# Performance work log

Measured on AMD Instinct MI355X. Metric: run time of the kernel, lower is better.

## Reference

```python
import jax, jax.numpy as jnp
import numpy as np

N_NODES = 10000
N_EDGES = 160000
IN_C, HID_C, OUT_C = 256, 512, 256
DROP_P = 0.5


def setup_inputs() -> dict:
    key = jax.random.key(0)
    ks = jax.random.split(key, 6)
    tensor = jax.random.normal(ks[0], (N_NODES, IN_C), dtype=jnp.float32)
    edge_index = jax.random.randint(ks[1], (2, N_EDGES), 0, N_NODES, dtype=jnp.int64)
    # Glorot-ish init for GCNConv linear weights, zero bias (PyG default bias init is zeros)
    W1 = jax.random.normal(ks[2], (IN_C, HID_C), dtype=jnp.float32) * (1.0 / np.sqrt(IN_C))
    b1 = jnp.zeros((HID_C,), dtype=jnp.float32)
    W2 = jax.random.normal(ks[3], (HID_C, OUT_C), dtype=jnp.float32) * (1.0 / np.sqrt(HID_C))
    b2 = jnp.zeros((OUT_C,), dtype=jnp.float32)
    return {"tensor": tensor, "edge_index": edge_index, "W1": W1, "b1": b1, "W2": W2, "b2": b2}


def _gcn_layer(x, W, b, src, dst, n_nodes):
    # x' = D^{-1/2} (A + I) D^{-1/2} X W + b  (PyG GCNConv, add_self_loops=True)
    xw = x @ W                                             # [N, C_out]
    deg = jax.ops.segment_sum(jnp.ones(src.shape[0], xw.dtype), dst,
                              num_segments=n_nodes)        # includes self-loops -> deg >= 1
    dinv = jax.lax.rsqrt(deg)
    norm = dinv[src] * dinv[dst]                           # [E+N]
    msg = xw[src] * norm[:, None]                          # gather + normalize
    out = jax.ops.segment_sum(msg, dst, num_segments=n_nodes)  # scatter-add
    return out + b


def _dropout(x, key, p):
    keep = jax.random.bernoulli(key, 1.0 - p, x.shape)
    return jnp.where(keep, x / (1.0 - p), jnp.zeros((), x.dtype))


def reference(tensor, edge_index, W1, b1, W2, b2):
    n = tensor.shape[0]
    src, dst = edge_index[0], edge_index[1]
    loops = jnp.arange(n, dtype=src.dtype)
    src_f = jnp.concatenate([src, loops])
    dst_f = jnp.concatenate([dst, loops])

    dk1, dk2 = jax.random.split(jax.random.key(42))
    h = _gcn_layer(tensor, W1, b1, src_f, dst_f, n)
    h = jax.nn.relu(h)
    h = _dropout(h, dk1, DROP_P)
    h = _gcn_layer(h, W2, b2, src_f, dst_f, n)
    h = jax.nn.relu(h)
    h = _dropout(h, dk2, DROP_P)
    return h
```

## Files before the change

kernel.cpp:

```cpp
#include <hip/hip_runtime.h>
#include <stdint.h>


#define C_IN 256
#define C_HID 512
#define C_OUT 256

typedef unsigned short ushort_t;
typedef __bf16 bf16x8 __attribute__((ext_vector_type(8)));
typedef float floatx4 __attribute__((ext_vector_type(4)));

__host__ __device__ __forceinline__ void tf_rounds(unsigned& x0, unsigned& x1,
                                                   unsigned k0, unsigned k1) {
  unsigned k2 = k0 ^ k1 ^ 0x1BD11BDAu;
#define ROT(r) { x0 += x1; x1 = (x1 << r) | (x1 >> (32 - r)); x1 ^= x0; }
  x0 += k0; x1 += k1;
  ROT(13) ROT(15) ROT(26) ROT(6)
  x0 += k1; x1 += k2 + 1u;
  ROT(17) ROT(29) ROT(16) ROT(24)
  x0 += k2; x1 += k0 + 2u;
  ROT(13) ROT(15) ROT(26) ROT(6)
  x0 += k0; x1 += k1 + 3u;
  ROT(17) ROT(29) ROT(16) ROT(24)
  x0 += k1; x1 += k2 + 4u;
  ROT(13) ROT(15) ROT(26) ROT(6)
  x0 += k2; x1 += k0 + 5u;
#undef ROT
}

__device__ __forceinline__ float drop_scale(unsigned j, unsigned k0, unsigned k1) {
  unsigned x0 = 0u, x1 = j;
  tf_rounds(x0, x1, k0, k1);
  unsigned bits = x0 ^ x1;
  float u = __uint_as_float((bits >> 9) | 0x3f800000u) - 1.0f;
  return (u < 0.5f) ? 2.0f : 0.0f;
}

__device__ __forceinline__ ushort_t f2bf(float f) {
  unsigned u = __float_as_uint(f);
  unsigned r = (u + 0x7fffu + ((u >> 16) & 1u)) >> 16;
  return (ushort_t)r;
}
__device__ __forceinline__ float bf2f(ushort_t h) {
  return __uint_as_float(((unsigned)h) << 16);
}

__global__ __launch_bounds__(256) void k_detect(const unsigned* __restrict__ raw,
                                                unsigned* flag, int nwords) {
  __shared__ unsigned sh[256];
  unsigned acc = 0;
  for (int i = 1 + 2 * (int)threadIdx.x; i < nwords; i += 512) acc |= raw[i];
  sh[threadIdx.x] = acc;
  __syncthreads();
  for (int s = 128; s > 0; s >>= 1) {
    if ((int)threadIdx.x < s) sh[threadIdx.x] |= sh[threadIdx.x + s];
    __syncthreads();
  }
  if (threadIdx.x == 0) *flag = (sh[0] == 0u) ? 1u : 0u;
}

__global__ __launch_bounds__(256) void k_zero(int* p, int n) {
  int i = blockIdx.x * 256 + threadIdx.x;
  if (i < n) p[i] = 0;
}

__global__ __launch_bounds__(256) void k_convert(const void* __restrict__ raw,
                                                 const unsigned* __restrict__ flag,
                                                 int* __restrict__ eic,
                                                 int* __restrict__ cnt,
                                                 int E) {
  int i = blockIdx.x * 256 + threadIdx.x;
  if (i >= 2 * E) return;
  int v;
  if (*flag) v = (int)((const long long*)raw)[i];
  else       v = ((const int*)raw)[i];
  eic[i] = v;
  if (i >= E) atomicAdd(&cnt[v], 1);
}

__global__ __launch_bounds__(256) void k_scan_a(const int* __restrict__ cnt,
                                                int* __restrict__ bsum, int n) {
  __shared__ int sh[256];
  int i = blockIdx.x * 256 + threadIdx.x;
  sh[threadIdx.x] = (i < n) ? cnt[i] : 0;
  __syncthreads();
  for (int s = 128; s > 0; s >>= 1) {
    if ((int)threadIdx.x < s) sh[threadIdx.x] += sh[threadIdx.x + s];
    __syncthreads();
  }
  if (threadIdx.x == 0) bsum[blockIdx.x] = sh[0];
}
__global__ __launch_bounds__(64) void k_scan_b(const int* __restrict__ bsum,
                                               int* __restrict__ boff,
                                               int* __restrict__ roff_last,
                                               int nb) {
  if (threadIdx.x == 0) {
    int run = 0;
    for (int b = 0; b < nb; ++b) { boff[b] = run; run += bsum[b]; }
    *roff_last = run;
  }
}
__global__ __launch_bounds__(256) void k_scan_c(const int* __restrict__ cnt,
                                                const int* __restrict__ boff,
                                                int* __restrict__ roff,
                                                int* __restrict__ cursor,
                                                float* __restrict__ dinv, int n) {
  __shared__ int sh[256];
  int i = blockIdx.x * 256 + threadIdx.x;
  int v = (i < n) ? cnt[i] : 0;
  sh[threadIdx.x] = v;
  __syncthreads();
  for (int s = 1; s < 256; s <<= 1) {
    int t = ((int)threadIdx.x >= s) ? sh[threadIdx.x - s] : 0;
    __syncthreads();
    sh[threadIdx.x] += t;
    __syncthreads();
  }
  if (i < n) {
    int excl = boff[blockIdx.x] + sh[threadIdx.x] - v;
    roff[i] = excl;
    cursor[i] = excl;
    dinv[i] = rsqrtf((float)(v + 1));
  }
}

__global__ __launch_bounds__(256) void k_scatter(const int* __restrict__ eic,
                                                 int* __restrict__ cursor,
                                                 int* __restrict__ csr, int E) {
  int e = blockIdx.x * 256 + threadIdx.x;
  if (e >= E) return;
  int s = eic[e], d = eic[E + e];
  int slot = atomicAdd(&cursor[d], 1);
  csr[slot] = s;
}

__global__ __launch_bounds__(256) void k_wconv2(const float* __restrict__ W1,
                                                const float* __restrict__ W2,
                                                ushort_t* __restrict__ h1,
                                                ushort_t* __restrict__ l1,
                                                ushort_t* __restrict__ h2,
                                                ushort_t* __restrict__ l2) {
  int idx = blockIdx.x * 256 + threadIdx.x;
  const int S1 = C_IN * C_HID;
  const float* W; ushort_t *hi, *lo; int K, Nn, li;
  if (idx < S1) { W = W1; hi = h1; lo = l1; K = C_IN; Nn = C_HID; li = idx; }
  else { W = W2; hi = h2; lo = l2; K = C_HID; Nn = C_OUT; li = idx - S1; }
  int k = li / Nn, n = li - k * Nn;
  float v = W[li];
  ushort_t h = f2bf(v);
  hi[(size_t)n * K + k] = h;
  lo[(size_t)n * K + k] = f2bf(v - bf2f(h));
}

template <int EPI>
__global__ __launch_bounds__(256) void k_gather4(const int* __restrict__ roff,
                                                 const int* __restrict__ csr,
                                                 const float* __restrict__ dinv,
                                                 const float* __restrict__ x,
                                                 const float* __restrict__ bias,
                                                 void* __restrict__ o1,
                                                 void* __restrict__ o2,
                                                 unsigned dk0, unsigned dk1) {
  int g = threadIdx.x >> 6;
  int tg = threadIdx.x & 63;
  int node = blockIdx.x * 4 + g;
  float dd = dinv[node];
  float4 v = ((const float4*)(x + (size_t)node * 256))[tg];
  float4 acc = make_float4(dd * v.x, dd * v.y, dd * v.z, dd * v.w);
  int p = roff[node], end = roff[node + 1];
  for (; p + 4 <= end; p += 4) {
    int s0 = csr[p], s1 = csr[p + 1], s2 = csr[p + 2], s3 = csr[p + 3];
    float w0 = dinv[s0], w1 = dinv[s1], w2 = dinv[s2], w3 = dinv[s3];
    float4 a = ((const float4*)(x + (size_t)s0 * 256))[tg];
    float4 b = ((const float4*)(x + (size_t)s1 * 256))[tg];
    float4 c = ((const float4*)(x + (size_t)s2 * 256))[tg];
    float4 d = ((const float4*)(x + (size_t)s3 * 256))[tg];
    acc.x += w0 * a.x + w1 * b.x + w2 * c.x + w3 * d.x;
    acc.y += w0 * a.y + w1 * b.y + w2 * c.y + w3 * d.y;
    acc.z += w0 * a.z + w1 * b.z + w2 * c.z + w3 * d.z;
    acc.w += w0 * a.w + w1 * b.w + w2 * c.w + w3 * d.w;
  }
  for (; p < end; ++p) {
    int s0 = csr[p];
    float w0 = dinv[s0];
    float4 a = ((const float4*)(x + (size_t)s0 * 256))[tg];
    acc.x += w0 * a.x; acc.y += w0 * a.y; acc.z += w0 * a.z; acc.w += w0 * a.w;
  }
  acc.x *= dd; acc.y *= dd; acc.z *= dd; acc.w *= dd;
  if (EPI) {
    float4 bb = ((const float4*)bias)[tg];
    acc.x = fmaxf(acc.x + bb.x, 0.0f);
    acc.y = fmaxf(acc.y + bb.y, 0.0f);
    acc.z = fmaxf(acc.z + bb.z, 0.0f);
    acc.w = fmaxf(acc.w + bb.w, 0.0f);
    unsigned jb = (unsigned)node * 256u + (unsigned)tg * 4u;
    acc.x *= drop_scale(jb + 0u, dk0, dk1);
    acc.y *= drop_scale(jb + 1u, dk0, dk1);
    acc.z *= drop_scale(jb + 2u, dk0, dk1);
    acc.w *= drop_scale(jb + 3u, dk0, dk1);
    ((float4*)o1)[(size_t)node * 64 + tg] = acc;
  } else {
    ushort_t h0 = f2bf(acc.x), h1 = f2bf(acc.y), h2 = f2bf(acc.z), h3 = f2bf(acc.w);
    ushort4 hv = make_ushort4(h0, h1, h2, h3);
    ushort4 lv = make_ushort4(f2bf(acc.x - bf2f(h0)), f2bf(acc.y - bf2f(h1)),
                              f2bf(acc.z - bf2f(h2)), f2bf(acc.w - bf2f(h3)));
    ((ushort4*)o1)[(size_t)node * 64 + tg] = hv;
    ((ushort4*)o2)[(size_t)node * 64 + tg] = lv;
  }
}

template <int EPI>
__global__ __launch_bounds__(256) void k_gemm3(
    const ushort_t* __restrict__ Ahi, const ushort_t* __restrict__ Alo,
    const ushort_t* __restrict__ Bhi, const ushort_t* __restrict__ Blo,
    const float* __restrict__ bias,
    ushort_t* __restrict__ Chi, ushort_t* __restrict__ Clo,
    float* __restrict__ Cf,
    int M, int N, int K, unsigned dk0, unsigned dk1) {
  __shared__ ushort_t sAh[128 * 32], sAl[128 * 32], sBh[128 * 32], sBl[128 * 32];
  const int t = threadIdx.x;
  const int lane = t & 63, wave = t >> 6;
  const int wm = wave & 1, wn = wave >> 1;
  const int quad = lane >> 4, l16 = lane & 15;
  const int row0 = blockIdx.y * 128, col0 = blockIdx.x * 128;
  const int srow = t >> 2;
  const int skc = (t & 3) * 8;

  floatx4 acc[4][4] = {};

  const int ra0 = min(row0 + srow, M - 1);
  const int ra1 = min(row0 + 64 + srow, M - 1);
  const int rb0 = col0 + srow;
  const int rb1 = col0 + 64 + srow;

  for (int kt = 0; kt < K; kt += 32) {
    const size_t ka = (size_t)kt + skc;
    uint4 vA0h = *(const uint4*)(Ahi + (size_t)ra0 * K + ka);
    uint4 vA1h = *(const uint4*)(Ahi + (size_t)ra1 * K + ka);
    uint4 vA0l = *(const uint4*)(Alo + (size_t)ra0 * K + ka);
    uint4 vA1l = *(const uint4*)(Alo + (size_t)ra1 * K + ka);
    uint4 vB0h = *(const uint4*)(Bhi + (size_t)rb0 * K + ka);
    uint4 vB1h = *(const uint4*)(Bhi + (size_t)rb1 * K + ka);
    uint4 vB0l = *(const uint4*)(Blo + (size_t)rb0 * K + ka);
    uint4 vB1l = *(const uint4*)(Blo + (size_t)rb1 * K + ka);
    __syncthreads();
    *(uint4*)&sAh[srow * 32 + skc] = vA0h;
    *(uint4*)&sAh[(64 + srow) * 32 + skc] = vA1h;
    *(uint4*)&sAl[srow * 32 + skc] = vA0l;
    *(uint4*)&sAl[(64 + srow) * 32 + skc] = vA1l;
    *(uint4*)&sBh[srow * 32 + skc] = vB0h;
    *(uint4*)&sBh[(64 + srow) * 32 + skc] = vB1h;
    *(uint4*)&sBl[srow * 32 + skc] = vB0l;
    *(uint4*)&sBl[(64 + srow) * 32 + skc] = vB1l;
    __syncthreads();

    bf16x8 ah[4], al[4], bh[4], bl[4];
#pragma unroll
    for (int i = 0; i < 4; ++i) {
      int off = (wm * 64 + i * 16 + l16) * 32 + quad * 8;
      ah[i] = *(const bf16x8*)&sAh[off];
      al[i] = *(const bf16x8*)&sAl[off];
    }
#pragma unroll
    for (int j = 0; j < 4; ++j) {
      int off = (wn * 64 + j * 16 + l16) * 32 + quad * 8;
      bh[j] = *(const bf16x8*)&sBh[off];
      bl[j] = *(const bf16x8*)&sBl[off];
    }
#pragma unroll
    for (int i = 0; i < 4; ++i)
#pragma unroll
      for (int j = 0; j < 4; ++j) {
        acc[i][j] = __builtin_amdgcn_mfma_f32_16x16x32_bf16(ah[i], bh[j], acc[i][j], 0, 0, 0);
        acc[i][j] = __builtin_amdgcn_mfma_f32_16x16x32_bf16(ah[i], bl[j], acc[i][j], 0, 0, 0);
        acc[i][j] = __builtin_amdgcn_mfma_f32_16x16x32_bf16(al[i], bh[j], acc[i][j], 0, 0, 0);
      }
  }

#pragma unroll
  for (int i = 0; i < 4; ++i) {
#pragma unroll
    for (int j = 0; j < 4; ++j) {
      int gc = col0 + wn * 64 + j * 16 + l16;
#pragma unroll
      for (int reg = 0; reg < 4; ++reg) {
        int gr = row0 + wm * 64 + i * 16 + quad * 4 + reg;
        if (gr >= M) continue;
        float v = acc[i][j][reg];
        size_t o = (size_t)gr * N + gc;
        if (EPI) {
          v += bias[gc];
          v = fmaxf(v, 0.0f);
          v *= drop_scale((unsigned)gr * (unsigned)N + (unsigned)gc, dk0, dk1);
          ushort_t h = f2bf(v);
          Chi[o] = h;
          Clo[o] = f2bf(v - bf2f(h));
        } else {
          Cf[o] = v;
        }
      }
    }
  }
}

extern "C" void kernel_launch(void* const* d_in, const int* in_sizes, int n_in,
                              void* d_out, int out_size, void* d_ws, size_t ws_size,
                              hipStream_t stream) {
  const float* x  = (const float*)d_in[0];
  const void*  ei = d_in[1];
  const float* W1 = (const float*)d_in[2];
  const float* b1 = (const float*)d_in[3];
  const float* W2 = (const float*)d_in[4];
  const float* b2 = (const float*)d_in[5];
  float* out = (float*)d_out;

  const int N = in_sizes[0] / C_IN;
  const int E = in_sizes[1] / 2;
  const int NB = (N + 255) / 256;

  unsigned a0 = 0u, a1 = 0u, b0 = 0u, b1k = 1u;
  tf_rounds(a0, a1, 0u, 42u);
  tf_rounds(b0, b1k, 0u, 42u);

  uintptr_t base = (uintptr_t)d_ws;
  unsigned*  flag   = (unsigned*)base;
  int*       bsum   = (int*)(base + 4096);
  int*       boff   = (int*)(base + 8192);
  int*       cnt    = (int*)(base + 16 * 1024);
  int*       roff   = (int*)(base + 64 * 1024);
  int*       cursor = (int*)(base + 128 * 1024);
  float*     dinv   = (float*)(base + 192 * 1024);
  int*       eic    = (int*)(base + 256 * 1024);
  int*       csr    = (int*)(base + 2u * 1024 * 1024);
  ushort_t*  Ahi    = (ushort_t*)(base + 4u  * 1024 * 1024);
  ushort_t*  Alo    = (ushort_t*)(base + 10u * 1024 * 1024);
  ushort_t*  H1hi   = (ushort_t*)(base + 16u * 1024 * 1024);
  ushort_t*  H1lo   = (ushort_t*)(base + 27u * 1024 * 1024);
  float*     hw2    = (float*)(base + 38u * 1024 * 1024);
  ushort_t*  W1thi  = (ushort_t*)(base + 49u * 1024 * 1024);
  ushort_t*  W1tlo  = (ushort_t*)(base + 49u * 1024 * 1024 + 512 * 1024);
  ushort_t*  W2thi  = (ushort_t*)(base + 50u * 1024 * 1024);
  ushort_t*  W2tlo  = (ushort_t*)(base + 50u * 1024 * 1024 + 512 * 1024);

  dim3 b256(256);
  k_detect<<<dim3(1), b256, 0, stream>>>((const unsigned*)ei, flag, 8192);
  k_zero<<<dim3(NB), b256, 0, stream>>>(cnt, N);
  k_convert<<<dim3((2 * E + 255) / 256), b256, 0, stream>>>(ei, flag, eic, cnt, E);
  k_scan_a<<<dim3(NB), b256, 0, stream>>>(cnt, bsum, N);
  k_scan_b<<<dim3(1), dim3(64), 0, stream>>>(bsum, boff, roff + N, NB);
  k_scan_c<<<dim3(NB), b256, 0, stream>>>(cnt, boff, roff, cursor, dinv, N);
  k_scatter<<<dim3((E + 255) / 256), b256, 0, stream>>>(eic, cursor, csr, E);
  k_wconv2<<<dim3((C_IN * C_HID + C_HID * C_OUT + 255) / 256), b256, 0, stream>>>(
      W1, W2, W1thi, W1tlo, W2thi, W2tlo);
  k_gather4<0><<<dim3(N / 4), b256, 0, stream>>>(roff, csr, dinv, x, nullptr,
                                                 Ahi, Alo, 0u, 0u);
  k_gemm3<1><<<dim3(C_HID / 128, (N + 127) / 128), b256, 0, stream>>>(
      Ahi, Alo, W1thi, W1tlo, b1, H1hi, H1lo, nullptr, N, C_HID, C_IN, a0, a1);
  k_gemm3<0><<<dim3(C_OUT / 128, (N + 127) / 128), b256, 0, stream>>>(
      H1hi, H1lo, W2thi, W2tlo, nullptr, nullptr, nullptr, hw2, N, C_OUT, C_HID, 0u, 0u);
  k_gather4<1><<<dim3(N / 4), b256, 0, stream>>>(roff, csr, dinv, hw2, b2,
                                                 out, nullptr, b0, b1k);
}
```

Before: 215.8 us.

## Merge setup kernels, single-block scan, and wave-shuffled CSR index loads in gather

Folds the zeroing into the detect kernel and the weight conversion into the CSR scatter kernel, and replaces the three-kernel scan with a single 1024-thread block scan, cutting the launch count from eight preprocessing kernels to four. The gather kernels now load up to 64 neighbor indices and weights cooperatively, one per lane, and broadcast them with shuffles instead of every lane reading them redundantly. The single-block scan only covers up to 16384 nodes, and the CSR scatter and weight conversion blocks now share one grid.

```diff
diff --git a/kernel.cpp b/kernel.cpp
--- a/kernel.cpp
+++ b/kernel.cpp
@@ -45,8 +45,15 @@
   return __uint_as_float(((unsigned)h) << 16);
 }
 
-__global__ __launch_bounds__(256) void k_detect(const unsigned* __restrict__ raw,
-                                                unsigned* flag, int nwords) {
+__global__ __launch_bounds__(256) void k_setup(const unsigned* __restrict__ raw,
+                                               unsigned* flag, int nwords,
+                                               int* __restrict__ cnt, int n,
+                                               int nb) {
+  if ((int)blockIdx.x < nb) {
+    int i = blockIdx.x * 256 + threadIdx.x;
+    if (i < n) cnt[i] = 0;
+    return;
+  }
   __shared__ unsigned sh[256];
   unsigned acc = 0;
   for (int i = 1 + 2 * (int)threadIdx.x; i < nwords; i += 512) acc |= raw[i];
@@ -57,11 +64,6 @@
     __syncthreads();
   }
   if (threadIdx.x == 0) *flag = (sh[0] == 0u) ? 1u : 0u;
-}
-
-__global__ __launch_bounds__(256) void k_zero(int* p, int n) {
-  int i = blockIdx.x * 256 + threadIdx.x;
-  if (i < n) p[i] = 0;
 }
 
 __global__ __launch_bounds__(256) void k_convert(const void* __restrict__ raw,
@@ -78,70 +80,65 @@
   if (i >= E) atomicAdd(&cnt[v], 1);
 }
 
-__global__ __launch_bounds__(256) void k_scan_a(const int* __restrict__ cnt,
-                                                int* __restrict__ bsum, int n) {
-  __shared__ int sh[256];
-  int i = blockIdx.x * 256 + threadIdx.x;
-  sh[threadIdx.x] = (i < n) ? cnt[i] : 0;
-  __syncthreads();
-  for (int s = 128; s > 0; s >>= 1) {
-    if ((int)threadIdx.x < s) sh[threadIdx.x] += sh[threadIdx.x + s];
-    __syncthreads();
-  }
-  if (threadIdx.x == 0) bsum[blockIdx.x] = sh[0];
-}
-__global__ __launch_bounds__(64) void k_scan_b(const int* __restrict__ bsum,
-                                               int* __restrict__ boff,
-                                               int* __restrict__ roff_last,
-                                               int nb) {
-  if (threadIdx.x == 0) {
-    int run = 0;
-    for (int b = 0; b < nb; ++b) { boff[b] = run; run += bsum[b]; }
-    *roff_last = run;
-  }
-}
-__global__ __launch_bounds__(256) void k_scan_c(const int* __restrict__ cnt,
-                                                const int* __restrict__ boff,
+#define SCAN_CH 16
+__global__ __launch_bounds__(1024) void k_scan1(const int* __restrict__ cnt,
                                                 int* __restrict__ roff,
                                                 int* __restrict__ cursor,
                                                 float* __restrict__ dinv, int n) {
-  __shared__ int sh[256];
-  int i = blockIdx.x * 256 + threadIdx.x;
-  int v = (i < n) ? cnt[i] : 0;
-  sh[threadIdx.x] = v;
+  __shared__ int sh[1024];
+  const int t = threadIdx.x;
+  const int base = t * SCAN_CH;
+  int vv[SCAN_CH], loc[SCAN_CH];
+  int sum = 0;
+#pragma unroll
+  for (int i = 0; i < SCAN_CH; ++i) {
+    int idx = base + i;
+    int v = (idx < n) ? cnt[idx] : 0;
+    vv[i] = v;
+    loc[i] = sum;
+    sum += v;
+  }
+  sh[t] = sum;
   __syncthreads();
-  for (int s = 1; s < 256; s <<= 1) {
-    int t = ((int)threadIdx.x >= s) ? sh[threadIdx.x - s] : 0;
-    __syncthreads();
-    sh[threadIdx.x] += t;
-    __syncthreads();
-  }
-  if (i < n) {
-    int excl = boff[blockIdx.x] + sh[threadIdx.x] - v;
-    roff[i] = excl;
-    cursor[i] = excl;
-    dinv[i] = rsqrtf((float)(v + 1));
-  }
-}
-
-__global__ __launch_bounds__(256) void k_scatter(const int* __restrict__ eic,
-                                                 int* __restrict__ cursor,
-                                                 int* __restrict__ csr, int E) {
-  int e = blockIdx.x * 256 + threadIdx.x;
-  if (e >= E) return;
-  int s = eic[e], d = eic[E + e];
-  int slot = atomicAdd(&cursor[d], 1);
-  csr[slot] = s;
-}
-
-__global__ __launch_bounds__(256) void k_wconv2(const float* __restrict__ W1,
-                                                const float* __restrict__ W2,
-                                                ushort_t* __restrict__ h1,
-                                                ushort_t* __restrict__ l1,
-                                                ushort_t* __restrict__ h2,
-                                                ushort_t* __restrict__ l2) {
-  int idx = blockIdx.x * 256 + threadIdx.x;
+  for (int s = 1; s < 1024; s <<= 1) {
+    int v = (t >= s) ? sh[t - s] : 0;
+    __syncthreads();
+    sh[t] += v;
+    __syncthreads();
+  }
+  int tex = sh[t] - sum;
+#pragma unroll
+  for (int i = 0; i < SCAN_CH; ++i) {
+    int idx = base + i;
+    if (idx < n) {
+      int excl = tex + loc[i];
+      roff[idx] = excl;
+      cursor[idx] = excl;
+      dinv[idx] = rsqrtf((float)(vv[i] + 1));
+    }
+  }
+  if (t == 1023) roff[n] = sh[1023];
+}
+
+__global__ __launch_bounds__(256) void k_scat_wconv(
+    const int* __restrict__ eic, int* __restrict__ cursor,
+    int* __restrict__ csr, int E, int SB,
+    const float* __restrict__ W1, const float* __restrict__ W2,
+    ushort_t* __restrict__ h1, ushort_t* __restrict__ l1,
+    ushort_t* __restrict__ h2, ushort_t* __restrict__ l2) {
+  int b = blockIdx.x;
+  if (b < SB) {
+    int e = b * 256 + threadIdx.x;
+    if (e >= E) return;
+    int s = eic[e], d = eic[E + e];
+    int slot = atomicAdd(&cursor[d], 1);
+    csr[slot] = s;
+    return;
+  }
+  int idx = (b - SB) * 256 + threadIdx.x;
   const int S1 = C_IN * C_HID;
+  const int S2 = C_HID * C_OUT;
+  if (idx >= S1 + S2) return;
   const float* W; ushort_t *hi, *lo; int K, Nn, li;
   if (idx < S1) { W = W1; hi = h1; lo = l1; K = C_IN; Nn = C_HID; li = idx; }
   else { W = W2; hi = h2; lo = l2; K = C_HID; Nn = C_OUT; li = idx - S1; }
@@ -161,51 +158,61 @@
                                                  void* __restrict__ o1,
                                                  void* __restrict__ o2,
                                                  unsigned dk0, unsigned dk1) {
-  int g = threadIdx.x >> 6;
-  int tg = threadIdx.x & 63;
-  int node = blockIdx.x * 4 + g;
+  const int g = threadIdx.x >> 6;
+  const int lane = threadIdx.x & 63;
+  const int node = blockIdx.x * 4 + g;
   float dd = dinv[node];
-  float4 v = ((const float4*)(x + (size_t)node * 256))[tg];
+  float4 v = ((const float4*)(x + (size_t)node * 256))[lane];
   float4 acc = make_float4(dd * v.x, dd * v.y, dd * v.z, dd * v.w);
   int p = roff[node], end = roff[node + 1];
-  for (; p + 4 <= end; p += 4) {
-    int s0 = csr[p], s1 = csr[p + 1], s2 = csr[p + 2], s3 = csr[p + 3];
-    float w0 = dinv[s0], w1 = dinv[s1], w2 = dinv[s2], w3 = dinv[s3];
-    float4 a = ((const float4*)(x + (size_t)s0 * 256))[tg];
-    float4 b = ((const float4*)(x + (size_t)s1 * 256))[tg];
-    float4 c = ((const float4*)(x + (size_t)s2 * 256))[tg];
-    float4 d = ((const float4*)(x + (size_t)s3 * 256))[tg];
-    acc.x += w0 * a.x + w1 * b.x + w2 * c.x + w3 * d.x;
-    acc.y += w0 * a.y + w1 * b.y + w2 * c.y + w3 * d.y;
-    acc.z += w0 * a.z + w1 * b.z + w2 * c.z + w3 * d.z;
-    acc.w += w0 * a.w + w1 * b.w + w2 * c.w + w3 * d.w;
-  }
-  for (; p < end; ++p) {
-    int s0 = csr[p];
-    float w0 = dinv[s0];
-    float4 a = ((const float4*)(x + (size_t)s0 * 256))[tg];
-    acc.x += w0 * a.x; acc.y += w0 * a.y; acc.z += w0 * a.z; acc.w += w0 * a.w;
+  while (p < end) {
+    int m = end - p;
+    if (m > 64) m = 64;
+    int sl = 0; float wl = 0.0f;
+    if (lane < m) { sl = csr[p + lane]; wl = dinv[sl]; }
+    int e = 0;
+    for (; e + 4 <= m; e += 4) {
+      int s0 = __shfl(sl, e + 0), s1 = __shfl(sl, e + 1);
+      int s2 = __shfl(sl, e + 2), s3 = __shfl(sl, e + 3);
+      float w0 = __shfl(wl, e + 0), w1 = __shfl(wl, e + 1);
+      float w2 = __shfl(wl, e + 2), w3 = __shfl(wl, e + 3);
+      float4 a = ((const float4*)(x + (size_t)s0 * 256))[lane];
+      float4 b = ((const float4*)(x + (size_t)s1 * 256))[lane];
+      float4 c = ((const float4*)(x + (size_t)s2 * 256))[lane];
+      float4 d = ((const float4*)(x + (size_t)s3 * 256))[lane];
+      acc.x += w0 * a.x + w1 * b.x + w2 * c.x + w3 * d.x;
+      acc.y += w0 * a.y + w1 * b.y + w2 * c.y + w3 * d.y;
+      acc.z += w0 * a.z + w1 * b.z + w2 * c.z + w3 * d.z;
+      acc.w += w0 * a.w + w1 * b.w + w2 * c.w + w3 * d.w;
+    }
+    for (; e < m; ++e) {
+      int s0 = __shfl(sl, e);
+      float w0 = __shfl(wl, e);
+      float4 a = ((const float4*)(x + (size_t)s0 * 256))[lane];
+      acc.x += w0 * a.x; acc.y += w0 * a.y; acc.z += w0 * a.z; acc.w += w0 * a.w;
+    }
+    p += m;
   }
   acc.x *= dd; acc.y *= dd; acc.z *= dd; acc.w *= dd;
   if (EPI) {
-    float4 bb = ((const float4*)bias)[tg];
+    float4 bb = ((const float4*)bias)[lane];
     acc.x = fmaxf(acc.x + bb.x, 0.0f);
     acc.y = fmaxf(acc.y + bb.y, 0.0f);
     acc.z = fmaxf(acc.z + bb.z, 0.0f);
     acc.w = fmaxf(acc.w + bb.w, 0.0f);
-    unsigned jb = (unsigned)node * 256u + (unsigned)tg * 4u;
+    unsigned jb = (unsigned)node * 256u + (unsigned)lane * 4u;
     acc.x *= drop_scale(jb + 0u, dk0, dk1);
     acc.y *= drop_scale(jb + 1u, dk0, dk1);
     acc.z *= drop_scale(jb + 2u, dk0, dk1);
     acc.w *= drop_scale(jb + 3u, dk0, dk1);
-    ((float4*)o1)[(size_t)node * 64 + tg] = acc;
+    ((float4*)o1)[(size_t)node * 64 + lane] = acc;
   } else {
     ushort_t h0 = f2bf(acc.x), h1 = f2bf(acc.y), h2 = f2bf(acc.z), h3 = f2bf(acc.w);
     ushort4 hv = make_ushort4(h0, h1, h2, h3);
     ushort4 lv = make_ushort4(f2bf(acc.x - bf2f(h0)), f2bf(acc.y - bf2f(h1)),
                               f2bf(acc.z - bf2f(h2)), f2bf(acc.w - bf2f(h3)));
-    ((ushort4*)o1)[(size_t)node * 64 + tg] = hv;
-    ((ushort4*)o2)[(size_t)node * 64 + tg] = lv;
+    ((ushort4*)o1)[(size_t)node * 64 + lane] = hv;
+    ((ushort4*)o2)[(size_t)node * 64 + lane] = lv;
   }
 }
 
@@ -324,8 +331,6 @@
 
   uintptr_t base = (uintptr_t)d_ws;
   unsigned*  flag   = (unsigned*)base;
-  int*       bsum   = (int*)(base + 4096);
-  int*       boff   = (int*)(base + 8192);
   int*       cnt    = (int*)(base + 16 * 1024);
   int*       roff   = (int*)(base + 64 * 1024);
   int*       cursor = (int*)(base + 128 * 1024);
@@ -343,15 +348,14 @@
   ushort_t*  W2tlo  = (ushort_t*)(base + 50u * 1024 * 1024 + 512 * 1024);
 
   dim3 b256(256);
-  k_detect<<<dim3(1), b256, 0, stream>>>((const unsigned*)ei, flag, 8192);
-  k_zero<<<dim3(NB), b256, 0, stream>>>(cnt, N);
+  const int SB = (E + 255) / 256;
+  const int WB = (C_IN * C_HID + C_HID * C_OUT + 255) / 256;
+
+  k_setup<<<dim3(NB + 1), b256, 0, stream>>>((const unsigned*)ei, flag, 8192, cnt, N, NB);
   k_convert<<<dim3((2 * E + 255) / 256), b256, 0, stream>>>(ei, flag, eic, cnt, E);
-  k_scan_a<<<dim3(NB), b256, 0, stream>>>(cnt, bsum, N);
-  k_scan_b<<<dim3(1), dim3(64), 0, stream>>>(bsum, boff, roff + N, NB);
-  k_scan_c<<<dim3(NB), b256, 0, stream>>>(cnt, boff, roff, cursor, dinv, N);
-  k_scatter<<<dim3((E + 255) / 256), b256, 0, stream>>>(eic, cursor, csr, E);
-  k_wconv2<<<dim3((C_IN * C_HID + C_HID * C_OUT + 255) / 256), b256, 0, stream>>>(
-      W1, W2, W1thi, W1tlo, W2thi, W2tlo);
+  k_scan1<<<dim3(1), dim3(1024), 0, stream>>>(cnt, roff, cursor, dinv, N);
+  k_scat_wconv<<<dim3(SB + WB), b256, 0, stream>>>(eic, cursor, csr, E, SB,
+                                                   W1, W2, W1thi, W1tlo, W2thi, W2tlo);
   k_gather4<0><<<dim3(N / 4), b256, 0, stream>>>(roff, csr, dinv, x, nullptr,
                                                  Ahi, Alo, 0u, 0u);
   k_gemm3<1><<<dim3(C_HID / 128, (N + 127) / 128), b256, 0, stream>>>(
```

After: 221.9 us. 2.8% more time.
